# Kernel tuning notes

Hardware: AMD Instinct MI355X
Metric: run time of the kernel (lower is better)

The kernel has to match this reference:

```python
import jax, jax.numpy as jnp
import numpy as np

NUM_HEADS = 4
HEAD_DIM = 64
IN_CH = 192
KERNEL_SIZES = (3, 5, 7, 9)  # per-head neighborhood size
NEG_INF = -1e30


def setup_inputs() -> dict:
    key = jax.random.key(0)
    k1, k2, k3 = jax.random.split(key, 3)
    x = jax.random.normal(k1, (8, IN_CH, 96, 96), dtype=jnp.float32)
    # QKV conv: out_channels = head_dim * num_heads * 3 = 768, 3x3, pad 1
    w_qkv = jax.random.normal(k2, (HEAD_DIM * NUM_HEADS * 3, IN_CH, 3, 3), dtype=jnp.float32) * 0.02
    b_qkv = jax.random.normal(k3, (HEAD_DIM * NUM_HEADS * 3,), dtype=jnp.float32) * 0.02
    return {"x": x, "w_qkv": w_qkv, "b_qkv": b_qkv}


def _neighborhood_attention(q, k, v, ksize):
    # q, k, v: [N, H, W, D]; KxK zero-padded neighborhood attention with
    # out-of-bounds positions masked out.
    N, H, W, D = q.shape
    pad = ksize // 2
    kp = jnp.pad(k, ((0, 0), (pad, pad), (pad, pad), (0, 0)))
    vp = jnp.pad(v, ((0, 0), (pad, pad), (pad, pad), (0, 0)))
    scale = 1.0 / np.sqrt(D).astype(np.float32)
    rows = jnp.arange(H)
    cols = jnp.arange(W)
    scores, masks = [], []
    for di in range(ksize):
        for dj in range(ksize):
            k_sh = kp[:, di:di + H, dj:dj + W, :]           # shifted keys
            scores.append(jnp.einsum('nhwd,nhwd->nhw', q, k_sh))
            rv = (rows + di - pad >= 0) & (rows + di - pad < H)   # [H]
            cv = (cols + dj - pad >= 0) & (cols + dj - pad < W)   # [W]
            masks.append(rv[:, None] & cv[None, :])               # [H, W]
    scores = jnp.stack(scores, axis=-1) * scale                   # [N,H,W,K2]
    mask = jnp.stack(masks, axis=-1)[None]                        # [1,H,W,K2]
    scores = jnp.where(mask, scores, NEG_INF)
    attn = jax.nn.softmax(scores, axis=-1)                        # [N,H,W,K2]
    out = jnp.zeros_like(q)
    t = 0
    for di in range(ksize):
        for dj in range(ksize):
            out = out + attn[..., t, None] * vp[:, di:di + H, dj:dj + W, :]
            t += 1
    return out  # [N,H,W,D]


def reference(x, w_qkv, b_qkv):
    # Dense QKV projection (Conv2d, stride 1, padding 1 == SAME for k=3)
    qkv = jax.lax.conv_general_dilated(
        x, w_qkv, window_strides=(1, 1), padding='SAME',
        dimension_numbers=('NCHW', 'OIHW', 'NCHW'))
    qkv = qkv + b_qkv[None, :, None, None]
    # transform_to_nhw1c: NCHW -> NHWC, then split channels into
    # num_heads blocks of 3*head_dim, each split into q, k, v.
    N, C, H, W = qkv.shape
    qkv = jnp.transpose(qkv, (0, 2, 3, 1)).reshape(N, H, W, NUM_HEADS, 3, HEAD_DIM)
    outs = []
    for h, ks in enumerate(KERNEL_SIZES):
        q = qkv[..., h, 0, :]
        k = qkv[..., h, 1, :]
        v = qkv[..., h, 2, :]
        o = _neighborhood_attention(q, k, v, ks)       # [N,H,W,D]
        outs.append(jnp.transpose(o, (0, 3, 1, 2)))    # transform_from_nhw1c -> NCHW
    return jnp.stack(outs, axis=0)  # [num_heads, N, D, H, W]
```

## Files before the change

### kernel.cpp

```cpp
#include <hip/hip_runtime.h>
#include <hip/hip_bf16.h>

#define NH 96
#define NW 96
#define NB 8
#define CIN 192
#define COUT 768
#define PH 98

typedef __attribute__((ext_vector_type(8))) unsigned short ushort8;
typedef __attribute__((ext_vector_type(8))) short bf16x8;
typedef __attribute__((ext_vector_type(4))) float f32x4;

static __device__ __forceinline__ unsigned short f2bf(float f) {
    unsigned int u = __float_as_uint(f);
    return (unsigned short)((u + 0x7fffu + ((u >> 16) & 1u)) >> 16);
}

typedef const __attribute__((address_space(1))) unsigned int gu32;
typedef __attribute__((address_space(3))) unsigned int lu32;
static __device__ __forceinline__ void gload16(const void* g, void* l) {
    __builtin_amdgcn_global_load_lds((gu32*)g, (lu32*)l, 16, 0, 0);
}

__global__ __launch_bounds__(256) void pack_x_kernel(
    const float* __restrict__ x, unsigned short* __restrict__ xp)
{
    __shared__ float tile[32][97];
    int bid = blockIdx.x;
    int ct = bid % 6; int y = (bid / 6) % NH; int n = bid / (6 * NH);
    int tid = threadIdx.x;
    int c0 = ct * 32;
    for (int i = tid; i < 32 * 96; i += 256) {
        int c = i / 96, xx = i % 96;
        tile[c][xx] = x[(((size_t)n * CIN + c0 + c) * NH + y) * NW + xx];
    }
    __syncthreads();
    for (int i = tid; i < 96 * 4; i += 256) {
        int xx = i >> 2, ch = i & 3;
        ushort8 pk;
#pragma unroll
        for (int j = 0; j < 8; ++j) pk[j] = f2bf(tile[ch * 8 + j][xx]);
        *(ushort8*)(xp + ((size_t)(n * PH + y + 1) * PH + xx + 1) * CIN + c0 + ch * 8) = pk;
    }
}

__global__ __launch_bounds__(256) void pack_w_kernel(
    const float* __restrict__ w, unsigned short* __restrict__ bw)
{
    __shared__ float ls[1728];
    int co = blockIdx.x; int tid = threadIdx.x;
    for (int i = tid; i < 1728; i += 256) ls[i] = w[(size_t)co * 1728 + i];
    __syncthreads();
    for (int i = tid; i < 1728; i += 256) {
        int sh = i / 192, ci = i % 192;
        bw[(size_t)co * 1728 + i] = f2bf(ls[ci * 9 + sh]);
    }
}

#define BUFSZ 24576

#define STAGE(S, BUF)                                                          \
    {                                                                          \
        int shift_ = (S) / 6, kk_ = (S) - shift_ * 6;                          \
        int aO_ = ((shift_ / 3) * PH + (shift_ % 3)) * CIN + kk_ * 32;         \
        int bO_ = (S) * 32;                                                    \
        gload16(srcA[0] + aO_, dstA[0] + (BUF));                               \
        gload16(srcA[1] + aO_, dstA[1] + (BUF));                               \
        _Pragma("unroll")                                                      \
        for (int i_ = 0; i_ < 4; ++i_)                                         \
            gload16(srcB[i_] + bO_, dstB[i_] + (BUF));                         \
    }

#define COMPUTE(CUR)                                                           \
    {                                                                          \
        bf16x8 af[8], bf[4];                                                   \
        _Pragma("unroll")                                                      \
        for (int m_ = 0; m_ < 8; ++m_)                                         \
            af[m_] = *(const bf16x8*)(smem + (CUR) + aoff[m_]);                \
        _Pragma("unroll")                                                      \
        for (int n_ = 0; n_ < 4; ++n_)                                         \
            bf[n_] = *(const bf16x8*)(smem + (CUR) + boff[n_]);                \
        __builtin_amdgcn_s_setprio(1);                                         \
        _Pragma("unroll")                                                      \
        for (int m_ = 0; m_ < 8; ++m_)                                         \
            _Pragma("unroll")                                                  \
            for (int n_ = 0; n_ < 4; ++n_)                                     \
                acc[m_][n_] = __builtin_amdgcn_mfma_f32_16x16x32_bf16(         \
                    af[m_], bf[n_], acc[m_][n_], 0, 0, 0);                     \
        __builtin_amdgcn_s_setprio(0);                                         \
    }

__global__ __launch_bounds__(256, 2) void conv_gemm_kernel(
    const unsigned short* __restrict__ xp, const unsigned short* __restrict__ bw,
    const float* __restrict__ bias, unsigned short* __restrict__ qkq,
    unsigned short* __restrict__ vt)
{
    __shared__ __align__(16) char smem[3 * BUFSZ];
    int bid = (blockIdx.x & 7) * 216 + (blockIdx.x >> 3);
    int brow = (bid / 3) * 128, bcol = (bid % 3) * 256;
    int tid = threadIdx.x, lane = tid & 63, wn = tid >> 6;

    const unsigned short* srcA[2];
    const unsigned short* srcB[4];
    char* dstA[2];
    char* dstB[4];
#pragma unroll
    for (int i = 0; i < 2; ++i) {
        int s = i * 256 + tid;
        int row = s >> 2, c = s & 3;
        int p = brow + row;
        int n = p / 9216; int rem = p - n * 9216;
        int y = rem / 96; int xx = rem - y * 96;
        int csw = (c ^ ((row >> 1) & 3)) << 3;
        srcA[i] = xp + ((size_t)(n * PH + y) * PH + xx) * CIN + csw;
        dstA[i] = smem + (i * 256 + (tid & ~63)) * 16;
    }
#pragma unroll
    for (int i = 0; i < 4; ++i) {
        int s = i * 256 + tid;
        int row = s >> 2, c = s & 3;
        int csw = (c ^ ((row >> 1) & 3)) << 3;
        srcB[i] = bw + (size_t)(bcol + row) * 1728 + csw;
        dstB[i] = smem + 8192 + (i * 256 + (tid & ~63)) * 16;
    }

    int aoff[8], boff[4];
#pragma unroll
    for (int m = 0; m < 8; ++m) {
        int rowA = m * 16 + (lane & 15);
        aoff[m] = rowA * 64 + (((lane >> 4) ^ ((rowA >> 1) & 3)) << 4);
    }
#pragma unroll
    for (int n = 0; n < 4; ++n) {
        int colB = wn * 64 + n * 16 + (lane & 15);
        boff[n] = 8192 + colB * 64 + (((lane >> 4) ^ ((colB >> 1) & 3)) << 4);
    }

    STAGE(0, 0);
    STAGE(1, BUFSZ);

    f32x4 acc[8][4] = {};

    for (int t = 0; t < 52; ++t) {
        asm volatile("s_waitcnt vmcnt(6)" ::: "memory");
        __builtin_amdgcn_s_barrier();
        STAGE(t + 2, ((t + 2) % 3) * BUFSZ);
        __builtin_amdgcn_sched_barrier(0);
        COMPUTE((t % 3) * BUFSZ);
    }
    asm volatile("s_waitcnt vmcnt(6)" ::: "memory");
    __builtin_amdgcn_s_barrier();
    COMPUTE((52 % 3) * BUFSZ);
    asm volatile("s_waitcnt vmcnt(0)" ::: "memory");
    __builtin_amdgcn_s_barrier();
    COMPUTE((53 % 3) * BUFSZ);

    __syncthreads();
    unsigned short* sc = (unsigned short*)smem;
    float bn[4];
#pragma unroll
    for (int n = 0; n < 4; ++n)
        bn[n] = bias[bcol + wn * 64 + n * 16 + (lane & 15)];
#pragma unroll
    for (int m = 0; m < 8; ++m)
#pragma unroll
        for (int n = 0; n < 4; ++n) {
            int col = wn * 64 + n * 16 + (lane & 15);
            int cabs = bcol + col;
            float scale = ((cabs % 192) < 64) ? 0.125f : 1.0f;
#pragma unroll
            for (int j = 0; j < 4; ++j) {
                int row = m * 16 + (lane >> 4) * 4 + j;
                sc[row * 256 + (col ^ ((row & 7) << 3))] =
                    f2bf((acc[m][n][j] + bn[n]) * scale);
            }
        }
    __syncthreads();
#pragma unroll
    for (int i = 0; i < 16; ++i) {
        int idx = i * 256 + tid;
        int row = idx >> 5, ch = idx & 31;
        int c0 = bcol + ch * 8;
        int r192 = c0 % 192;
        if (r192 < 128) {
            ushort8 pk = *(const ushort8*)(sc + row * 256 + ((ch * 8) ^ ((row & 7) << 3)));
            *(ushort8*)(qkq + (size_t)(brow + row) * 512 + (c0 / 192) * 128 + r192) = pk;
        }
    }
    int nblk = brow / 9216;
    int prem = brow - nblk * 9216;
#pragma unroll
    for (int h = 0; h < 4; ++h) {
        int lc = h * 192 + 128 - bcol;
        if (lc < 0 || lc > 192) continue;
        unsigned short* vth = vt + (size_t)h * 4718592;
#pragma unroll
        for (int it = 0; it < 4; ++it) {
            int i = it * 256 + tid;
            int d = i & 63, pxb = i >> 6;
            ushort8 pk;
#pragma unroll
            for (int j = 0; j < 8; ++j) {
                int px = pxb * 8 + j;
                pk[j] = sc[px * 256 + ((lc + d) ^ ((px & 7) << 3))];
            }
            *(ushort8*)(vth + ((size_t)(nblk * 64 + d)) * 9216 + prem + pxb * 8) = pk;
        }
    }
}

template<int KS>
static __device__ __forceinline__ void na_body(
    const unsigned short* __restrict__ qkq, const unsigned short* __restrict__ vt,
    float* __restrict__ out, int head, int bid)
{
    constexpr int PAD = KS / 2;
    __shared__ float sO[64][97];
    int y = bid % 96, n = bid / 96;
    int tid = threadIdx.x;
    int wv = tid >> 6, lane = tid & 63;
    int g = lane >> 4, pix = lane & 15;
    int x0 = wv * 16;
    int x = x0 + pix;
    int W = x0 - 8;

    size_t qbase = ((size_t)((n * 96 + y) * 96 + x)) * 512 + (size_t)head * 128;
    bf16x8 qf0 = *(const bf16x8*)(qkq + qbase + g * 8);
    bf16x8 qf1 = *(const bf16x8*)(qkq + qbase + 32 + g * 8);

    f32x4 s[KS][2];
#pragma unroll
    for (int di = 0; di < KS; ++di)
#pragma unroll
        for (int kt = 0; kt < 2; ++kt)
#pragma unroll
            for (int r = 0; r < 4; ++r) s[di][kt][r] = -1e30f;

#pragma unroll
    for (int di = 0; di < KS; ++di) {
        int iy = y + di - PAD;
        if (iy < 0 || iy >= 96) continue;
#pragma unroll
        for (int kt = 0; kt < 2; ++kt) {
            int kix_l = W + kt * 16 + pix;
            int ixc = min(max(kix_l, 0), 95);
            size_t kbase = ((size_t)((n * 96 + iy) * 96 + ixc)) * 512
                           + (size_t)head * 128 + 64;
            bf16x8 kf0 = *(const bf16x8*)(qkq + kbase + g * 8);
            bf16x8 kf1 = *(const bf16x8*)(qkq + kbase + 32 + g * 8);
            f32x4 t = {};
            t = __builtin_amdgcn_mfma_f32_16x16x32_bf16(kf0, qf0, t, 0, 0, 0);
            t = __builtin_amdgcn_mfma_f32_16x16x32_bf16(kf1, qf1, t, 0, 0, 0);
#pragma unroll
            for (int r = 0; r < 4; ++r) {
                int kix = W + kt * 16 + g * 4 + r;
                bool valid = ((unsigned)(kix - x + PAD) <= (unsigned)(2 * PAD)) &&
                             ((unsigned)kix < 96u);
                s[di][kt][r] = valid ? t[r] : -1e30f;
            }
        }
    }

    float m = -3.0e38f;
#pragma unroll
    for (int di = 0; di < KS; ++di)
#pragma unroll
        for (int kt = 0; kt < 2; ++kt)
#pragma unroll
            for (int r = 0; r < 4; ++r) m = fmaxf(m, s[di][kt][r]);
    m = fmaxf(m, __shfl_xor(m, 16, 64));
    m = fmaxf(m, __shfl_xor(m, 32, 64));
    float l = 0.f;
#pragma unroll
    for (int di = 0; di < KS; ++di)
#pragma unroll
        for (int kt = 0; kt < 2; ++kt)
#pragma unroll
            for (int r = 0; r < 4; ++r) {
                float p = __expf(s[di][kt][r] - m);
                s[di][kt][r] = p;
                l += p;
            }
    l += __shfl_xor(l, 16, 64);
    l += __shfl_xor(l, 32, 64);

    f32x4 O[4] = {};
    int addrA = ((2 * (g & 1)) * 16 + pix) * 4;
    int addrB = addrA + 64;
    bool kthi = (g >> 1) != 0;
#pragma unroll
    for (int di = 0; di < KS; ++di) {
        int iy = y + di - PAD;
        if (iy < 0 || iy >= 96) continue;
        unsigned int w0[2], w1[2];
#pragma unroll
        for (int kt = 0; kt < 2; ++kt) {
            asm("v_cvt_pk_bf16_f32 %0, %1, %2"
                : "=v"(w0[kt]) : "v"(s[di][kt][0]), "v"(s[di][kt][1]));
            asm("v_cvt_pk_bf16_f32 %0, %1, %2"
                : "=v"(w1[kt]) : "v"(s[di][kt][2]), "v"(s[di][kt][3]));
        }
        int a0 = __builtin_amdgcn_ds_bpermute(addrA, (int)w0[0]);
        int b0 = __builtin_amdgcn_ds_bpermute(addrA, (int)w0[1]);
        int a1 = __builtin_amdgcn_ds_bpermute(addrA, (int)w1[0]);
        int b1 = __builtin_amdgcn_ds_bpermute(addrA, (int)w1[1]);
        int a2 = __builtin_amdgcn_ds_bpermute(addrB, (int)w0[0]);
        int b2 = __builtin_amdgcn_ds_bpermute(addrB, (int)w0[1]);
        int a3 = __builtin_amdgcn_ds_bpermute(addrB, (int)w1[0]);
        int b3 = __builtin_amdgcn_ds_bpermute(addrB, (int)w1[1]);
        union { int u[4]; bf16x8 v; } pa;
        pa.u[0] = kthi ? b0 : a0;
        pa.u[1] = kthi ? b1 : a1;
        pa.u[2] = kthi ? b2 : a2;
        pa.u[3] = kthi ? b3 : a3;
#pragma unroll
        for (int dc = 0; dc < 4; ++dc) {
            long voff = ((long)((n * 64 + dc * 16 + pix) * 96 + iy)) * 96 + (W + g * 8);
            bf16x8 vf = *(const bf16x8*)(vt + voff);
            O[dc] = __builtin_amdgcn_mfma_f32_16x16x32_bf16(pa.v, vf, O[dc], 0, 0, 0);
        }
    }

    float linv = 1.0f / l;
    float linvj[4];
#pragma unroll
    for (int j = 0; j < 4; ++j)
        linvj[j] = __uint_as_float((unsigned)__builtin_amdgcn_ds_bpermute(
            (4 * g + j) * 4, (int)__float_as_uint(linv)));
#pragma unroll
    for (int dc = 0; dc < 4; ++dc)
#pragma unroll
        for (int j = 0; j < 4; ++j)
            sO[dc * 16 + pix][x0 + g * 4 + j] = O[dc][j] * linvj[j];
    __syncthreads();
    for (int i = tid; i < 1536; i += 384) {
        int d = i / 24, xq = i % 24;
        float4 v4 = { sO[d][xq * 4], sO[d][xq * 4 + 1],
                      sO[d][xq * 4 + 2], sO[d][xq * 4 + 3] };
        *(float4*)(out + ((size_t)(head * 8 + n) * 64 + d) * 9216
                   + y * 96 + xq * 4) = v4;
    }
}

__global__ __launch_bounds__(384, 3) void na_mfma_all(
    const unsigned short* __restrict__ qkq, const unsigned short* __restrict__ vt,
    float* __restrict__ out)
{
    int head = blockIdx.x / 768;
    int bid = blockIdx.x % 768;
    switch (head) {
        case 0: na_body<3>(qkq, vt,               out, 0, bid); break;
        case 1: na_body<5>(qkq, vt + 4718592,     out, 1, bid); break;
        case 2: na_body<7>(qkq, vt + 2 * 4718592, out, 2, bid); break;
        default: na_body<9>(qkq, vt + 3 * 4718592, out, 3, bid); break;
    }
}

extern "C" void kernel_launch(void* const* d_in, const int* in_sizes, int n_in,
                              void* d_out, int out_size, void* d_ws, size_t ws_size,
                              hipStream_t stream) {
    const float* x  = (const float*)d_in[0];
    const float* w  = (const float*)d_in[1];
    const float* b  = (const float*)d_in[2];
    float* out = (float*)d_out;

    unsigned short* qkq  = (unsigned short*)d_ws;
    unsigned short* vt   = (unsigned short*)((char*)d_ws + 75497472);
    unsigned short* xpad = (unsigned short*)((char*)d_ws + 113246208);
    unsigned short* bw   = (unsigned short*)((char*)d_ws + 142749696);

    hipMemsetAsync(xpad, 0, 29503488, stream);
    pack_x_kernel<<<NB * NH * 6, 256, 0, stream>>>(x, xpad);
    pack_w_kernel<<<COUT, 256, 0, stream>>>(w, bw);
    conv_gemm_kernel<<<1728, 256, 0, stream>>>(xpad, bw, b, qkq, vt);

    na_mfma_all<<<4 * 768, 384, 0, stream>>>(qkq, vt, out);
}
```

Measured before the change: 369.5 us.

## Stage neighborhood K rows through LDS with triple-buffered async loads

The attention kernel now prefetches each K row for the current image row into a swizzled LDS buffer using async global-to-LDS loads. It keeps three buffers so loads for row di+2 overlap compute on row di, with waitcnt and barrier between steps. This replaces the per-lane scattered global K loads. Block-to-head mapping also changes to interleave heads so the light and heavy kernel sizes are mixed across the grid. It adds 36KB of LDS per block and a barrier per row, which may limit occupancy.

```diff
diff --git a/kernel.cpp b/kernel.cpp
--- a/kernel.cpp
+++ b/kernel.cpp
@@ -213,10 +213,10 @@
 template<int KS>
 static __device__ __forceinline__ void na_body(
     const unsigned short* __restrict__ qkq, const unsigned short* __restrict__ vt,
-    float* __restrict__ out, int head, int bid)
+    float* __restrict__ out, int head, int bid, char* nsm)
 {
     constexpr int PAD = KS / 2;
-    __shared__ float sO[64][97];
+    float (*sO)[97] = (float(*)[97])nsm;
     int y = bid % 96, n = bid / 96;
     int tid = threadIdx.x;
     int wv = tid >> 6, lane = tid & 63;
@@ -228,6 +228,24 @@
     size_t qbase = ((size_t)((n * 96 + y) * 96 + x)) * 512 + (size_t)head * 128;
     bf16x8 qf0 = *(const bf16x8*)(qkq + qbase + g * 8);
     bf16x8 qf1 = *(const bf16x8*)(qkq + qbase + 32 + g * 8);
+    asm volatile("s_waitcnt vmcnt(0)" ::: "memory");
+
+    const size_t hoff = (size_t)head * 128 + 64;
+#define STAGEK(DI, BUF)                                                        \
+    {                                                                          \
+        int iy_ = min(max(y + (DI) - PAD, 0), 95);                             \
+        size_t rb_ = ((size_t)((n * 96 + iy_) * 96)) * 512 + hoff;             \
+        _Pragma("unroll")                                                      \
+        for (int i_ = 0; i_ < 2; ++i_) {                                       \
+            int ch_ = i_ * 384 + tid;                                          \
+            int xx_ = ch_ >> 3, c8_ = (ch_ & 7) ^ (xx_ & 7);                   \
+            gload16(qkq + rb_ + (size_t)xx_ * 512 + c8_ * 8,                   \
+                    nsm + (BUF) * 12288 + (i_ * 384 + (tid & ~63)) * 16);      \
+        }                                                                      \
+    }
+
+    STAGEK(0, 0);
+    STAGEK(1, 1);
 
     f32x4 s[KS][2];
 #pragma unroll
@@ -239,16 +257,20 @@
 
 #pragma unroll
     for (int di = 0; di < KS; ++di) {
+        if (di < KS - 1) asm volatile("s_waitcnt vmcnt(2)" ::: "memory");
+        else             asm volatile("s_waitcnt vmcnt(0)" ::: "memory");
+        __builtin_amdgcn_s_barrier();
+        if (di + 2 < KS) STAGEK(di + 2, (di + 2) % 3);
         int iy = y + di - PAD;
         if (iy < 0 || iy >= 96) continue;
+        const char* kb = nsm + (di % 3) * 12288;
 #pragma unroll
         for (int kt = 0; kt < 2; ++kt) {
             int kix_l = W + kt * 16 + pix;
             int ixc = min(max(kix_l, 0), 95);
-            size_t kbase = ((size_t)((n * 96 + iy) * 96 + ixc)) * 512
-                           + (size_t)head * 128 + 64;
-            bf16x8 kf0 = *(const bf16x8*)(qkq + kbase + g * 8);
-            bf16x8 kf1 = *(const bf16x8*)(qkq + kbase + 32 + g * 8);
+            const char* kr = kb + ixc * 128;
+            bf16x8 kf0 = *(const bf16x8*)(kr + ((g ^ (ixc & 7)) << 4));
+            bf16x8 kf1 = *(const bf16x8*)(kr + (((4 + g) ^ (ixc & 7)) << 4));
             f32x4 t = {};
             t = __builtin_amdgcn_mfma_f32_16x16x32_bf16(kf0, qf0, t, 0, 0, 0);
             t = __builtin_amdgcn_mfma_f32_16x16x32_bf16(kf1, qf1, t, 0, 0, 0);
@@ -328,6 +350,7 @@
     for (int j = 0; j < 4; ++j)
         linvj[j] = __uint_as_float((unsigned)__builtin_amdgcn_ds_bpermute(
             (4 * g + j) * 4, (int)__float_as_uint(linv)));
+    __syncthreads();
 #pragma unroll
     for (int dc = 0; dc < 4; ++dc)
 #pragma unroll
@@ -347,13 +370,14 @@
     const unsigned short* __restrict__ qkq, const unsigned short* __restrict__ vt,
     float* __restrict__ out)
 {
-    int head = blockIdx.x / 768;
-    int bid = blockIdx.x % 768;
+    __shared__ __align__(16) char nsm[36864];
+    int head = blockIdx.x & 3;
+    int bid = blockIdx.x >> 2;
     switch (head) {
-        case 0: na_body<3>(qkq, vt,               out, 0, bid); break;
-        case 1: na_body<5>(qkq, vt + 4718592,     out, 1, bid); break;
-        case 2: na_body<7>(qkq, vt + 2 * 4718592, out, 2, bid); break;
-        default: na_body<9>(qkq, vt + 3 * 4718592, out, 3, bid); break;
+        case 0: na_body<3>(qkq, vt,               out, 0, bid, nsm); break;
+        case 1: na_body<5>(qkq, vt + 4718592,     out, 1, bid, nsm); break;
+        case 2: na_body<7>(qkq, vt + 2 * 4718592, out, 2, bid, nsm); break;
+        default: na_body<9>(qkq, vt + 3 * 4718592, out, 3, bid, nsm); break;
     }
 }
 
```

New measurement: 364.8 us. No clear change (-1.3%).
